# Optimization experiments

Measured on AMD Instinct MI355X. Metric: run time of the kernel, lower is better.

Reference implementation:

```python
import jax, jax.numpy as jnp
import numpy as np

B, T, D, H, L = 2, 1000, 768, 12, 2
DK = D // H
MLP_HID = D * 1  # mlp_ratio = 1
WIDTHS = [7, 15, 31, 63, 127, 255, 7, 15, 31, 63, 127, 255]


def _band_mask():
    # diagonal_mask(seq_len, mask_width): True = blocked (outside the diagonal band)
    i = np.arange(T)[:, None]
    j = np.arange(T)[None, :]
    m = np.stack([np.abs(i - j) > (w // 2) for w in WIDTHS], 0)  # (H, T, T)
    return jnp.asarray(m)


def _rel_pos_emb():
    # espnet-style RelPositionalEncoding: rel positions T-1 .. -(T-1), shape (2T-1, D)
    pos = jnp.arange(T - 1, -T, -1, dtype=jnp.float32)
    div = jnp.exp(jnp.arange(0, D, 2, dtype=jnp.float32) * (-np.log(10000.0) / D))
    ang = pos[:, None] * div[None, :]
    return jnp.stack([jnp.sin(ang), jnp.cos(ang)], -1).reshape(2 * T - 1, D)


def setup_inputs() -> dict:
    key = jax.random.key(0)
    ks = iter(jax.random.split(key, 32))
    rn = lambda sh, s=0.02: jax.random.normal(next(ks), sh, jnp.float32) * s
    return {
        "x": jax.random.normal(next(ks), (B, T, D), jnp.float32),
        "mask": _band_mask(),
        "ln1_g": jnp.ones((L, D)), "ln1_b": jnp.zeros((L, D)),
        "wq": rn((L, D, D)), "bq": jnp.zeros((L, D)),
        "wk": rn((L, D, D)), "bk": jnp.zeros((L, D)),
        "wv": rn((L, D, D)), "bv": jnp.zeros((L, D)),
        "wo": rn((L, D, D)), "bo": jnp.zeros((L, D)),
        "wpos": rn((L, D, D)),
        "pbu": rn((L, H, DK)), "pbv": rn((L, H, DK)),
        "ln2_g": jnp.ones((L, D)), "ln2_b": jnp.zeros((L, D)),
        "w1": rn((L, D, MLP_HID)), "b1": jnp.zeros((L, MLP_HID)),
        "w2": rn((L, MLP_HID, D)), "b2": jnp.zeros((L, D)),
    }


def _ln(x, g, b):
    m = jnp.mean(x, -1, keepdims=True)
    v = jnp.var(x, -1, keepdims=True)
    return (x - m) * jax.lax.rsqrt(v + 1e-5) * g + b


def _rel_shift(x):
    # x: (b, h, t, 2t-1) -> shifted so column s corresponds to rel pos (t-1 - s + row offset)
    b, h, t, n = x.shape
    x = jnp.pad(x, ((0, 0), (0, 0), (0, 0), (1, 0)))        # (b,h,t,2t)
    x = x.reshape(b, h, n + 1, t)[:, :, 1:, :].reshape(b, h, t, n)
    return x[..., :t]


def _forward(x, mask, p):
    (ln1_g, ln1_b, wq, bq, wk, bk, wv, bv, wo, bo,
     wpos, pbu, pbv, ln2_g, ln2_b, w1, b1, w2, b2) = p
    pe = _rel_pos_emb()                                      # (2T-1, D)
    x = x * jnp.asarray(np.sqrt(D), x.dtype)                 # xscale in RelPositionalEncoding
    neg = jnp.asarray(-1e30, x.dtype)
    inv_sqrt_dk = 1.0 / np.sqrt(DK)
    for l in range(L):
        h = _ln(x, ln1_g[l], ln1_b[l])
        q = (h @ wq[l] + bq[l]).reshape(B, T, H, DK)
        k = (h @ wk[l] + bk[l]).reshape(B, T, H, DK)
        v = (h @ wv[l] + bv[l]).reshape(B, T, H, DK)
        pp = (pe @ wpos[l]).reshape(2 * T - 1, H, DK)        # pos projection (no bias)
        ac = jnp.einsum('bthd,bshd->bhts', q + pbu[l], k)    # content term
        bd = _rel_shift(jnp.einsum('bthd,nhd->bhtn', q + pbv[l], pp))  # position term
        s = (ac + bd) * inv_sqrt_dk
        s = jnp.where(mask[None], neg, s)                    # per-head diagonal band mask
        a = jax.nn.softmax(s, axis=-1)
        o = jnp.einsum('bhts,bshd->bthd', a, v).reshape(B, T, D) @ wo[l] + bo[l]
        x = x + o
        h2 = _ln(x, ln2_g[l], ln2_b[l])
        x = x + (jax.nn.gelu(h2 @ w1[l] + b1[l], approximate=False) @ w2[l] + b2[l])
    return x


def reference(x, mask, ln1_g, ln1_b, wq, bq, wk, bk, wv, bv, wo, bo, wpos, pbu, pbv, ln2_g, ln2_b, w1, b1, w2, b2):
    return _forward(x, mask, (ln1_g, ln1_b, wq, bq, wk, bk, wv, bv, wo, bo,
                              wpos, pbu, pbv, ln2_g, ln2_b, w1, b1, w2, b2))
```

## Files before the change

kernel.cpp:

```cpp
#include <hip/hip_runtime.h>

#define TT 1000
#define BB 2
#define DD 768
#define HH 12
#define DK 64
#define LL 2
#define WELEM 589824
#define PEROWS 255
#define VTP 1312
#define PPL 195840

typedef __bf16 bf16x8 __attribute__((ext_vector_type(8)));
typedef float floatx4 __attribute__((ext_vector_type(4)));

__device__ __constant__ int HALFW[12] = {3,7,15,31,63,127,3,7,15,31,63,127};
__device__ __constant__ int HORD[12]  = {5,11,4,10,3,9,2,8,1,7,0,6};


__device__ __forceinline__ float b2f(unsigned short u){
    union { unsigned int i; float f; } x; x.i = ((unsigned int)u) << 16; return x.f;
}
__device__ __forceinline__ unsigned short f2b(float f){
    union { float f; unsigned int i; } x; x.f = f;
    unsigned int i = x.i;
    i += 0x7fffu + ((i >> 16) & 1u);
    return (unsigned short)(i >> 16);
}
__device__ __forceinline__ void gload16(const void* g, void* l){
    __builtin_amdgcn_global_load_lds(
        (const __attribute__((address_space(1))) void*)g,
        (__attribute__((address_space(3))) void*)l, 16, 0, 0);
}

__global__ __launch_bounds__(256)
void prep_kernel(const float* s0, const float* s1, const float* s2, const float* s3,
                 const float* s4, const float* s5, const float* s6,
                 unsigned short* __restrict__ dst,
                 const float* __restrict__ x, float* __restrict__ xc,
                 unsigned short* __restrict__ pe,
                 const float* __restrict__ lg0, const float* __restrict__ lb0,
                 unsigned short* __restrict__ ln0out){
    int z = blockIdx.z;
    int tid = threadIdx.x;
    if (z < 14){
        const float* srcs[7] = {s0,s1,s2,s3,s4,s5,s6};
        const float* src = srcs[z % 7] + (size_t)(z / 7)*WELEM;
        unsigned short* d = dst + (size_t)z*WELEM;
        int k0 = blockIdx.x*64, n0 = blockIdx.y*64;
        __shared__ __align__(16) unsigned short tile[64][72];
        int r = tid >> 2, c = tid & 3;
        const float4* sp = (const float4*)(src + (size_t)(k0+r)*DD + n0 + c*16);
        float4 f0 = sp[0], f1 = sp[1], f2 = sp[2], f3 = sp[3];
        unsigned short u[16];
        u[0]=f2b(f0.x); u[1]=f2b(f0.y); u[2]=f2b(f0.z); u[3]=f2b(f0.w);
        u[4]=f2b(f1.x); u[5]=f2b(f1.y); u[6]=f2b(f1.z); u[7]=f2b(f1.w);
        u[8]=f2b(f2.x); u[9]=f2b(f2.y); u[10]=f2b(f2.z); u[11]=f2b(f2.w);
        u[12]=f2b(f3.x); u[13]=f2b(f3.y); u[14]=f2b(f3.z); u[15]=f2b(f3.w);
        *(int4*)&tile[r][c*16]   = *(int4*)&u[0];
        *(int4*)&tile[r][c*16+8] = *(int4*)&u[8];
        __syncthreads();
        unsigned short tmp[16];
        #pragma unroll
        for (int i=0;i<16;++i) tmp[i] = tile[c*16+i][r];
        int4* dp = (int4*)(d + (size_t)(n0+r)*DD + k0 + c*16);
        dp[0] = *(int4*)&tmp[0];
        dp[1] = *(int4*)&tmp[8];
    } else if (z == 14){
        int bid = blockIdx.y*12 + blockIdx.x;
        int wv = tid>>6, lane = tid&63;
        const float SCL = 27.712812921102035f;
        #pragma unroll
        for (int it = 0; it < 4; ++it){
            int rr = it*4 + wv;
            if (rr < 14){
                int row = bid*14 + rr;
                if (row < 2000){
                    const float4* xr = (const float4*)x + (size_t)row*192;
                    float4* xcr = (float4*)xc + (size_t)row*192;
                    float4 vv[3];
                    float s = 0.f, ss = 0.f;
                    #pragma unroll
                    for (int j=0;j<3;++j){
                        float4 vq = xr[lane + 64*j];
                        vq.x *= SCL; vq.y *= SCL; vq.z *= SCL; vq.w *= SCL;
                        vv[j] = vq;
                        s  += vq.x+vq.y+vq.z+vq.w;
                        ss += vq.x*vq.x+vq.y*vq.y+vq.z*vq.z+vq.w*vq.w;
                        xcr[lane + 64*j] = vq;
                    }
                    #pragma unroll
                    for (int o=1;o<64;o<<=1){ s += __shfl_xor(s,o); ss += __shfl_xor(ss,o); }
                    float mean = s*(1.0f/768.0f);
                    float var  = ss*(1.0f/768.0f) - mean*mean;
                    float inv  = 1.0f/sqrtf(var + 1e-5f);
                    unsigned short* orow = ln0out + (size_t)row*768;
                    #pragma unroll
                    for (int j=0;j<3;++j){
                        int i0 = (lane + 64*j)*4;
                        unsigned short o4[4];
                        o4[0] = f2b((vv[j].x-mean)*inv*lg0[i0]   + lb0[i0]);
                        o4[1] = f2b((vv[j].y-mean)*inv*lg0[i0+1] + lb0[i0+1]);
                        o4[2] = f2b((vv[j].z-mean)*inv*lg0[i0+2] + lb0[i0+2]);
                        o4[3] = f2b((vv[j].w-mean)*inv*lg0[i0+3] + lb0[i0+3]);
                        *(unsigned long long*)&orow[i0] = *(unsigned long long*)o4;
                    }
                }
            }
        }
    } else {
        int bid = blockIdx.y*12 + blockIdx.x;
        #pragma unroll
        for (int rr = 0; rr < 2; ++rr){
            int row = bid*2 + rr;
            if (row < PEROWS){
                float pos = (float)(127 - row);
                int i = tid;
                float dv = expf((float)(2*i) * (-9.210340371976184f / 768.0f));
                float ang = pos * dv;
                pe[(size_t)row*DD + 2*i]   = f2b(sinf(ang));
                pe[(size_t)row*DD + 2*i+1] = f2b(cosf(ang));
                if (tid < 128){
                    int j = 256 + tid;
                    float dv2 = expf((float)(2*j) * (-9.210340371976184f / 768.0f));
                    float an2 = pos * dv2;
                    pe[(size_t)row*DD + 2*j]   = f2b(sinf(an2));
                    pe[(size_t)row*DD + 2*j+1] = f2b(cosf(an2));
                }
            }
        }
    }
}

__global__ __launch_bounds__(256)
void ln_kernel(const float* __restrict__ x, const float* __restrict__ g,
               const float* __restrict__ bb, unsigned short* __restrict__ out){
    int row = blockIdx.x;
    const float* xr = x + (size_t)row*DD;
    int tid = threadIdx.x;
    float v0 = xr[tid], v1 = xr[tid+256], v2 = xr[tid+512];
    float s = v0+v1+v2, ss = v0*v0+v1*v1+v2*v2;
    #pragma unroll
    for (int o=1;o<64;o<<=1){ s += __shfl_xor(s,o); ss += __shfl_xor(ss,o); }
    __shared__ float rs[4], rss[4];
    int wv = tid>>6, lane = tid&63;
    if (lane==0){ rs[wv]=s; rss[wv]=ss; }
    __syncthreads();
    s  = rs[0]+rs[1]+rs[2]+rs[3];
    ss = rss[0]+rss[1]+rss[2]+rss[3];
    float mean = s * (1.0f/768.0f);
    float var  = ss * (1.0f/768.0f) - mean*mean;
    float inv  = 1.0f / sqrtf(var + 1e-5f);
    unsigned short* orow = out + (size_t)row*DD;
    #pragma unroll
    for (int kk=0;kk<3;++kk){
        int i = tid + 256*kk;
        float v = (kk==0?v0:(kk==1?v1:v2));
        orow[i] = f2b((v - mean)*inv*g[i] + bb[i]);
    }
}

#define GEMM_GL64(A_, Bt_, M0_, n0_, M_)                                        \
    int tid = threadIdx.x;                                                      \
    int m0 = (M0_);                                                             \
    int wv = tid>>6, lane = tid&63;                                             \
    int quad = lane>>4, l16 = lane&15;                                          \
    floatx4 acc[4];                                                             \
    _Pragma("unroll")                                                           \
    for (int ni=0;ni<4;++ni) acc[ni] = (floatx4){0.f,0.f,0.f,0.f};              \
    {                                                                           \
      int rl0 = wv*16 + (lane>>3);                                              \
      int rl1 = rl0 + 8;                                                        \
      int gc  = (lane&7) ^ (lane>>3);                                           \
      int ra0 = m0 + rl0; if (ra0 > (M_)-1) ra0 = (M_)-1;                       \
      int ra1 = m0 + rl1; if (ra1 > (M_)-1) ra1 = (M_)-1;                       \
      const char* gA0 = (const char*)(A_)  + (size_t)ra0*1536 + gc*16;          \
      const char* gA1 = (const char*)(A_)  + (size_t)ra1*1536 + gc*16;          \
      const char* gB0 = (const char*)(Bt_) + (size_t)((n0_)+rl0)*1536 + gc*16;  \
      const char* gB1 = (const char*)(Bt_) + (size_t)((n0_)+rl1)*1536 + gc*16;  \
      char* shB = (char*)sh;                                                    \
      int ld0 = (2*wv)*1024, ld1 = (2*wv+1)*1024;                               \
      int arow = (16*wv + l16)*64;                                              \
      int sw8  = l16 & 7;                                                       \
      int cq0 = (quad ^ sw8)*8;                                                 \
      int cq1 = ((4|quad) ^ sw8)*8;                                             \
      gload16(gA0, shB + ld0);                                                  \
      gload16(gA1, shB + ld1);                                                  \
      gload16(gB0, shB + 8192 + ld0);                                           \
      gload16(gB1, shB + 8192 + ld1);                                           \
      for (int s=0; s<12; ++s){                                                 \
        if (s < 11){                                                            \
          char* nb = shB + ((s+1)&1)*16384;                                     \
          int off = (s+1)*128;                                                  \
          gload16(gA0 + off, nb + ld0);                                         \
          gload16(gA1 + off, nb + ld1);                                         \
          gload16(gB0 + off, nb + 8192 + ld0);                                  \
          gload16(gB1 + off, nb + 8192 + ld1);                                  \
          asm volatile("s_waitcnt vmcnt(4)" ::: "memory");                      \
        } else {                                                                \
          asm volatile("s_waitcnt vmcnt(0)" ::: "memory");                      \
        }                                                                       \
        __builtin_amdgcn_s_barrier();                                           \
        __builtin_amdgcn_sched_barrier(0);                                      \
        const unsigned short* cA = sh + (s&1)*8192;                             \
        const unsigned short* cB = cA + 4096;                                   \
        _Pragma("unroll")                                                       \
        for (int kh=0; kh<2; ++kh){                                             \
          int cq = kh ? cq1 : cq0;                                              \
          bf16x8 af = *(const bf16x8*)&cA[arow + cq];                           \
          _Pragma("unroll")                                                     \
          for (int ni=0; ni<4; ++ni){                                           \
            bf16x8 bfv = *(const bf16x8*)&cB[ni*1024 + l16*64 + cq];            \
            acc[ni] = __builtin_amdgcn_mfma_f32_16x16x32_bf16(af, bfv, acc[ni], 0,0,0); \
          }                                                                     \
        }                                                                       \
        __builtin_amdgcn_sched_barrier(0);                                      \
        __builtin_amdgcn_s_barrier();                                           \
      }                                                                         \
    }

#define GEMM_GL64_3B(A_, Bt_, M0_, n0_, M_)                                     \
    int tid = threadIdx.x;                                                      \
    int m0 = (M0_);                                                             \
    int wv = tid>>6, lane = tid&63;                                             \
    int quad = lane>>4, l16 = lane&15;                                          \
    floatx4 acc[4];                                                             \
    _Pragma("unroll")                                                           \
    for (int ni=0;ni<4;++ni) acc[ni] = (floatx4){0.f,0.f,0.f,0.f};              \
    {                                                                           \
      int rl0 = wv*16 + (lane>>3);                                              \
      int rl1 = rl0 + 8;                                                        \
      int gc  = (lane&7) ^ (lane>>3);                                           \
      int ra0 = m0 + rl0; if (ra0 > (M_)-1) ra0 = (M_)-1;                       \
      int ra1 = m0 + rl1; if (ra1 > (M_)-1) ra1 = (M_)-1;                       \
      const char* gA0 = (const char*)(A_)  + (size_t)ra0*1536 + gc*16;          \
      const char* gA1 = (const char*)(A_)  + (size_t)ra1*1536 + gc*16;          \
      const char* gB0 = (const char*)(Bt_) + (size_t)((n0_)+rl0)*1536 + gc*16;  \
      const char* gB1 = (const char*)(Bt_) + (size_t)((n0_)+rl1)*1536 + gc*16;  \
      char* shB = (char*)sh;                                                    \
      int ld0 = (2*wv)*1024, ld1 = (2*wv+1)*1024;                               \
      int arow = (16*wv + l16)*64;                                              \
      int sw8  = l16 & 7;                                                       \
      int cq0 = (quad ^ sw8)*8;                                                 \
      int cq1 = ((4|quad) ^ sw8)*8;                                             \
      gload16(gA0, shB + ld0);                                                  \
      gload16(gA1, shB + ld1);                                                  \
      gload16(gB0, shB + 8192 + ld0);                                           \
      gload16(gB1, shB + 8192 + ld1);                                           \
      gload16(gA0 + 128, shB + 16384 + ld0);                                    \
      gload16(gA1 + 128, shB + 16384 + ld1);                                    \
      gload16(gB0 + 128, shB + 16384 + 8192 + ld0);                             \
      gload16(gB1 + 128, shB + 16384 + 8192 + ld1);                             \
      for (int s=0; s<12; ++s){                                                 \
        if (s < 11) asm volatile("s_waitcnt vmcnt(4)" ::: "memory");            \
        else        asm volatile("s_waitcnt vmcnt(0)" ::: "memory");            \
        __builtin_amdgcn_s_barrier();                                           \
        __builtin_amdgcn_sched_barrier(0);                                      \
        if (s < 10){                                                            \
          char* nb = shB + ((s+2)%3)*16384;                                     \
          int off = (s+2)*128;                                                  \
          gload16(gA0 + off, nb + ld0);                                         \
          gload16(gA1 + off, nb + ld1);                                         \
          gload16(gB0 + off, nb + 8192 + ld0);                                  \
          gload16(gB1 + off, nb + 8192 + ld1);                                  \
        }                                                                       \
        __builtin_amdgcn_sched_barrier(0);                                      \
        const unsigned short* cA = sh + (s%3)*8192;                             \
        const unsigned short* cB = cA + 4096;                                   \
        _Pragma("unroll")                                                       \
        for (int kh=0; kh<2; ++kh){                                             \
          int cq = kh ? cq1 : cq0;                                              \
          bf16x8 af = *(const bf16x8*)&cA[arow + cq];                           \
          _Pragma("unroll")                                                     \
          for (int ni=0; ni<4; ++ni){                                           \
            bf16x8 bfv = *(const bf16x8*)&cB[ni*1024 + l16*64 + cq];            \
            acc[ni] = __builtin_amdgcn_mfma_f32_16x16x32_bf16(af, bfv, acc[ni], 0,0,0); \
          }                                                                     \
        }                                                                       \
        __builtin_amdgcn_sched_barrier(0);                                      \
      }                                                                         \
    }

template<int MODE>
__global__ __launch_bounds__(256)
void gemm_kernel(const unsigned short* __restrict__ A, const unsigned short* __restrict__ Bt,
                 const float* __restrict__ bias, unsigned short* __restrict__ outb,
                 float* __restrict__ resid, int M){
    __shared__ __align__(16) unsigned short sh[24576];
    int n0 = blockIdx.y*64;
    GEMM_GL64_3B(A, Bt, blockIdx.x*64, n0, M)
    float bfv_[4];
    #pragma unroll
    for (int ni=0;ni<4;++ni) bfv_[ni] = bias ? bias[n0 + 16*ni + l16] : 0.0f;
    #pragma unroll
    for (int rr=0;rr<4;++rr){
        int row = m0 + 16*wv + 4*quad + rr;
        if (row >= M) continue;
        #pragma unroll
        for (int ni=0;ni<4;++ni){
            int col = n0 + 16*ni + l16;
            float v = acc[ni][rr] + bfv_[ni];
            if (MODE == 1)      outb[(size_t)row*768 + col] = f2b(0.5f*v*(1.0f + erff(v*0.70710678118654752f)));
            else                resid[(size_t)row*768 + col] += v;
        }
    }
}

__global__ __launch_bounds__(256)
void gemm_qkv_kernel(const unsigned short* __restrict__ A, const unsigned short* __restrict__ Bt,
                     const float* __restrict__ bq, const float* __restrict__ bk, const float* __restrict__ bv,
                     unsigned short* __restrict__ qout, unsigned short* __restrict__ kout,
                     unsigned short* __restrict__ vout,
                     const unsigned short* __restrict__ peA, const unsigned short* __restrict__ posBt,
                     unsigned short* __restrict__ ppout){
    __shared__ __align__(16) unsigned short sh[16384];
    int bid = blockIdx.x;
    if (bid < 1152){
        int ny = bid >> 5;
        int n0 = ny * 64;
        GEMM_GL64(A, Bt, (bid & 31)*64, n0, 2000)
        int sec = ny / 12;
        int col0 = n0 - sec*768;
        int h = col0 >> 6;
        const float* bias = (sec==0) ? bq : (sec==1) ? bk : bv;
        float bfv_[4];
        #pragma unroll
        for (int ni=0;ni<4;++ni) bfv_[ni] = bias[col0 + 16*ni + l16];
        if (sec != 2){
            unsigned short* outp = (sec==0) ? qout : kout;
            #pragma unroll
            for (int rr=0;rr<4;++rr){
                int row = m0 + 16*wv + 4*quad + rr;
                if (row >= 2000) continue;
                int b = row / TT, tl = row - b*TT;
                #pragma unroll
                for (int ni=0;ni<4;++ni){
                    int d = 16*ni + l16;
                    outp[(((size_t)(b*HH + h))*TT + tl)*DK + d] = f2b(acc[ni][rr] + bfv_[ni]);
                }
            }
        } else {
            #pragma unroll
            for (int rr=0;rr<4;++rr){
                int rt = 16*wv + 4*quad + rr;
                #pragma unroll
                for (int ni=0;ni<4;++ni)
                    sh[rt*66 + 16*ni + l16] = f2b(acc[ni][rr] + bfv_[ni]);
            }
            __syncthreads();
            #pragma unroll
            for (int it=0; it<16; ++it){
                int idx = it*256 + tid;
                int d = idx >> 6, rt = idx & 63;
                int row = m0 + rt;
                if (row < 2000){
                    int b = row / TT, tl = row - b*TT;
                    vout[(((size_t)(b*HH + h))*DK + d)*VTP + tl + 128] = sh[rt*66 + d];
                }
            }
        }
    } else {
        int pid = bid - 1152;
        int pz = pid / 48, rem = pid % 48;
        int pn0 = (rem >> 2) * 64;
        const unsigned short* Bt_ = posBt + (size_t)pz*7*WELEM;
        unsigned short* outb_ = ppout + (size_t)pz*PPL;
        GEMM_GL64(peA, Bt_, (rem & 3)*64, pn0, PEROWS)
        #pragma unroll
        for (int rr=0;rr<4;++rr){
            int row = m0 + 16*wv + 4*quad + rr;
            if (row >= PEROWS) continue;
            #pragma unroll
            for (int ni=0;ni<4;++ni){
                int col = pn0 + 16*ni + l16;
                int h = col >> 6, d = col & 63;
                outb_[((size_t)h*PEROWS + row)*DK + d] = f2b(acc[ni][rr]);
            }
        }
    }
}

__global__ __launch_bounds__(256)
void attn_kernel(const unsigned short* __restrict__ q, const unsigned short* __restrict__ k,
                 const unsigned short* __restrict__ vT, const unsigned short* __restrict__ pp,
                 const float* __restrict__ pbu, const float* __restrict__ pbv,
                 unsigned short* __restrict__ out){
    int b = blockIdx.y, h = HORD[blockIdx.z];
    int t0 = blockIdx.x * 16;
    int w2 = HALFW[h];
    int tid = threadIdx.x;
    int wv = tid >> 6, lane = tid & 63;
    int l16 = lane & 15, quad = lane >> 4;

    const unsigned short* qB = q  + ((size_t)(b*HH + h))*TT*DK;
    const unsigned short* kB = k  + ((size_t)(b*HH + h))*TT*DK;
    const unsigned short* vB = vT + ((size_t)(b*HH + h))*DK*VTP;
    const unsigned short* pB = pp + (size_t)h*PEROWS*DK;

    __shared__ __align__(16) float bd[16*260];
    __shared__ __align__(16) unsigned short pl[16*328];
    __shared__ float sms[4][16];

    int tq = t0 + l16; if (tq > TT-1) tq = TT-1;
    union { int4 i; unsigned short u[8]; } r0, r1;
    r0.i = *(const int4*)(qB + (size_t)tq*DK + quad*8);
    r1.i = *(const int4*)(qB + (size_t)tq*DK + 32 + quad*8);
    const float* pu = pbu + h*DK + quad*8;
    const float* pv = pbv + h*DK + quad*8;
    union { unsigned short u[8]; bf16x8 v; } qu0, qu1, qv0, qv1;
    #pragma unroll
    for (int i=0;i<8;++i){
        float a0 = b2f(r0.u[i]), a1 = b2f(r1.u[i]);
        qu0.u[i] = f2b(a0 + pu[i]);
        qu1.u[i] = f2b(a1 + pu[32+i]);
        qv0.u[i] = f2b(a0 + pv[i]);
        qv1.u[i] = f2b(a1 + pv[32+i]);
    }

    int Nn = 2*w2 + 1;
    int ntiles = (Nn + 15) >> 4;
    for (int ti = wv; ti < ntiles; ti += 4){
        int n = 127 - w2 + ti*16 + l16; if (n > PEROWS-1) n = PEROWS-1;
        const unsigned short* pr = pB + (size_t)n*DK + quad*8;
        bf16x8 pb0 = *(const bf16x8*)pr;
        bf16x8 pb1 = *(const bf16x8*)(pr + 32);
        floatx4 a = {0.f,0.f,0.f,0.f};
        a = __builtin_amdgcn_mfma_f32_16x16x32_bf16(qv0.v, pb0, a, 0,0,0);
        a = __builtin_amdgcn_mfma_f32_16x16x32_bf16(qv1.v, pb1, a, 0,0,0);
        #pragma unroll
        for (int r=0;r<4;++r) bd[(quad*4+r)*260 + ti*16 + l16] = a[r];
    }
    for (int i = tid; i < 16*328/4; i += 256)
        ((unsigned long long*)pl)[i] = 0ULL;
    __syncthreads();

    int Ns = 2*w2 + 16;
    int stiles = (Ns + 15) >> 4;
    int s_lo = t0 - w2;
    float scv[5][4];
    #pragma unroll
    for (int ii = 0; ii < 5; ++ii){
        int ti = wv + ii*4;
        if (ti < stiles){
            int s = s_lo + ti*16 + l16;
            int sc = s < 0 ? 0 : (s > TT-1 ? TT-1 : s);
            const unsigned short* kr = kB + (size_t)sc*DK + quad*8;
            bf16x8 kb0 = *(const bf16x8*)kr;
            bf16x8 kb1 = *(const bf16x8*)(kr + 32);
            floatx4 a = {0.f,0.f,0.f,0.f};
            a = __builtin_amdgcn_mfma_f32_16x16x32_bf16(qu0.v, kb0, a, 0,0,0);
            a = __builtin_amdgcn_mfma_f32_16x16x32_bf16(qu1.v, kb1, a, 0,0,0);
            #pragma unroll
            for (int r=0;r<4;++r){
                int row = quad*4 + r;
                int nrel = ti*16 + l16 - row;
                bool ok = (nrel >= 0) && (nrel <= 2*w2) && (s >= 0) && (s <= TT-1);
                int idx = row*260 + nrel;
                idx = idx < 0 ? 0 : (idx > 16*260-1 ? 16*260-1 : idx);
                float bdv = bd[idx];
                scv[ii][r] = ok ? (a[r] + bdv) * 0.125f : -1e30f;
            }
        } else {
            #pragma unroll
            for (int r=0;r<4;++r) scv[ii][r] = -1e30f;
        }
    }

    float sm[4] = {0.f,0.f,0.f,0.f};
    #pragma unroll
    for (int ii = 0; ii < 5; ++ii){
        int ti = wv + ii*4;
        if (ti < stiles){
            int pad_base = (t0 - w2) - ((t0 - w2) & ~31);
            #pragma unroll
            for (int r=0;r<4;++r){
                float e = __expf(scv[ii][r]);
                sm[r] += e;
                pl[(quad*4+r)*328 + pad_base + ti*16 + l16] = f2b(e);
            }
        }
    }
    #pragma unroll
    for (int off=1; off<16; off<<=1){
        #pragma unroll
        for (int r=0;r<4;++r) sm[r] += __shfl_xor(sm[r], off);
    }
    if (l16 == 0){
        #pragma unroll
        for (int r=0;r<4;++r) sms[wv][quad*4+r] = sm[r];
    }
    __syncthreads();

    int s_lo2 = t0 - w2;
    int s0a = s_lo2 & ~31;
    int pad_lo = s_lo2 - s0a;
    int ktiles = (pad_lo + Ns + 31) >> 5;

    floatx4 oacc = {0.f,0.f,0.f,0.f};
    for (int kt = 0; kt < ktiles; ++kt){
        bf16x8 pa = *(const bf16x8*)&pl[l16*328 + kt*32 + quad*8];
        int sidx = s0a + kt*32 + quad*8 + 128;
        bf16x8 vb = *(const bf16x8*)(vB + (size_t)(wv*16 + l16)*VTP + sidx);
        oacc = __builtin_amdgcn_mfma_f32_16x16x32_bf16(pa, vb, oacc, 0,0,0);
    }
    #pragma unroll
    for (int r=0;r<4;++r){
        int row = quad*4 + r;
        float sum = sms[0][row] + sms[1][row] + sms[2][row] + sms[3][row];
        float rinv = sum > 0.f ? 1.0f/sum : 0.0f;
        int t = t0 + row;
        if (t <= TT-1)
            out[(((size_t)(b*TT + t))*HH + h)*DK + wv*16 + l16] = f2b(oacc[r] * rinv);
    }
}

extern "C" void kernel_launch(void* const* d_in, const int* in_sizes, int n_in,
                              void* d_out, int out_size, void* d_ws, size_t ws_size,
                              hipStream_t stream){
    const float* x    = (const float*)d_in[0];
    const float* ln1g = (const float*)d_in[2];
    const float* ln1b = (const float*)d_in[3];
    const float* wq   = (const float*)d_in[4];
    const float* bq   = (const float*)d_in[5];
    const float* wk   = (const float*)d_in[6];
    const float* bk   = (const float*)d_in[7];
    const float* wvv  = (const float*)d_in[8];
    const float* bv   = (const float*)d_in[9];
    const float* wo   = (const float*)d_in[10];
    const float* bo   = (const float*)d_in[11];
    const float* wpos = (const float*)d_in[12];
    const float* pbu  = (const float*)d_in[13];
    const float* pbv  = (const float*)d_in[14];
    const float* ln2g = (const float*)d_in[15];
    const float* ln2b = (const float*)d_in[16];
    const float* w1   = (const float*)d_in[17];
    const float* b1   = (const float*)d_in[18];
    const float* w2   = (const float*)d_in[19];
    const float* b2   = (const float*)d_in[20];

    const int NTOK = BB*TT;

    float* x_cur = (float*)d_out;

    char* ws = (char*)d_ws;
    unsigned short* qbuf  = (unsigned short*)(ws);
    unsigned short* kbuf  = (unsigned short*)(ws + 3072000);
    unsigned short* vTbuf = (unsigned short*)(ws + 6144000);
    unsigned short* hbuf  = (unsigned short*)(ws + 10174464);
    unsigned short* ppbuf = (unsigned short*)(ws + 13246464);
    unsigned short* pebuf = (unsigned short*)(ws + 14029824);
    unsigned short* wtbuf = (unsigned short*)(ws + 14421504);
    #define WT(t_,l_) (wtbuf + (size_t)((l_)*7 + (t_))*WELEM)

    dim3 blk(256);
    prep_kernel<<<dim3(12,12,16), blk, 0, stream>>>(wq, wk, wvv, wo, wpos, w1, w2,
                                                    wtbuf, x, x_cur, pebuf,
                                                    ln1g, ln1b, hbuf);

    dim3 gBig(32, 12);
    dim3 gAttn(63, BB, HH);

    for (int l = 0; l < LL; ++l){
        long dl = (long)l*DD;
        long pl_ = (long)l*HH*DK;

        if (l == 1)
            ln_kernel<<<NTOK, blk, 0, stream>>>(x_cur, ln1g + dl, ln1b + dl, hbuf);

        int nqkv = (l == 0) ? 1248 : 1152;
        gemm_qkv_kernel<<<dim3(nqkv), blk, 0, stream>>>(hbuf, WT(0,l), bq + dl, bk + dl, bv + dl,
                                                        qbuf, kbuf, vTbuf,
                                                        pebuf, WT(4,0), ppbuf);

        attn_kernel<<<gAttn, blk, 0, stream>>>(qbuf, kbuf, vTbuf, ppbuf + (size_t)l*PPL,
                                               pbu + pl_, pbv + pl_, hbuf);

        gemm_kernel<2><<<gBig, blk, 0, stream>>>(hbuf, WT(3,l), bo + dl, nullptr, x_cur, NTOK);

        ln_kernel<<<NTOK, blk, 0, stream>>>(x_cur, ln2g + dl, ln2b + dl, hbuf);
        gemm_kernel<1><<<gBig, blk, 0, stream>>>(hbuf, WT(5,l), b1 + dl, qbuf, nullptr, NTOK);
        gemm_kernel<2><<<gBig, blk, 0, stream>>>(qbuf, WT(6,l), b2 + dl, nullptr, x_cur, NTOK);
    }
}
```

Before: 276.7 us.

## Fold LayerNorm2 into residual GEMM epilogue and FC1 weights via row stats

```diff
diff --git a/kernel.cpp b/kernel.cpp
--- a/kernel.cpp
+++ b/kernel.cpp
@@ -40,7 +40,8 @@
                  const float* __restrict__ x, float* __restrict__ xc,
                  unsigned short* __restrict__ pe,
                  const float* __restrict__ lg0, const float* __restrict__ lb0,
-                 unsigned short* __restrict__ ln0out){
+                 unsigned short* __restrict__ ln0out,
+                 const float* __restrict__ g2){
     int z = blockIdx.z;
     int tid = threadIdx.x;
     if (z < 14){
@@ -52,6 +53,13 @@
         int r = tid >> 2, c = tid & 3;
         const float4* sp = (const float4*)(src + (size_t)(k0+r)*DD + n0 + c*16);
         float4 f0 = sp[0], f1 = sp[1], f2 = sp[2], f3 = sp[3];
+        if (z % 7 == 5){
+            float g = g2[(size_t)(z/7)*DD + k0 + r];
+            f0.x*=g; f0.y*=g; f0.z*=g; f0.w*=g;
+            f1.x*=g; f1.y*=g; f1.z*=g; f1.w*=g;
+            f2.x*=g; f2.y*=g; f2.z*=g; f2.w*=g;
+            f3.x*=g; f3.y*=g; f3.z*=g; f3.w*=g;
+        }
         unsigned short u[16];
         u[0]=f2b(f0.x); u[1]=f2b(f0.y); u[2]=f2b(f0.z); u[3]=f2b(f0.w);
         u[4]=f2b(f1.x); u[5]=f2b(f1.y); u[6]=f2b(f1.z); u[7]=f2b(f1.w);
@@ -285,23 +293,57 @@
 __global__ __launch_bounds__(256)
 void gemm_kernel(const unsigned short* __restrict__ A, const unsigned short* __restrict__ Bt,
                  const float* __restrict__ bias, unsigned short* __restrict__ outb,
-                 float* __restrict__ resid, int M){
+                 float* __restrict__ resid, int M,
+                 float* __restrict__ stats, unsigned short* __restrict__ xbf,
+                 const float* __restrict__ uv, const float* __restrict__ cv){
     __shared__ __align__(16) unsigned short sh[24576];
     int n0 = blockIdx.y*64;
     GEMM_GL64_3B(A, Bt, blockIdx.x*64, n0, M)
     float bfv_[4];
     #pragma unroll
     for (int ni=0;ni<4;++ni) bfv_[ni] = bias ? bias[n0 + 16*ni + l16] : 0.0f;
-    #pragma unroll
-    for (int rr=0;rr<4;++rr){
-        int row = m0 + 16*wv + 4*quad + rr;
-        if (row >= M) continue;
-        #pragma unroll
-        for (int ni=0;ni<4;++ni){
-            int col = n0 + 16*ni + l16;
-            float v = acc[ni][rr] + bfv_[ni];
-            if (MODE == 1)      outb[(size_t)row*768 + col] = f2b(0.5f*v*(1.0f + erff(v*0.70710678118654752f)));
-            else                resid[(size_t)row*768 + col] += v;
+    if (MODE == 1){
+        float un[4], cn[4];
+        #pragma unroll
+        for (int ni=0;ni<4;++ni){ int col = n0 + 16*ni + l16; un[ni] = uv[col]; cn[ni] = cv[col]; }
+        #pragma unroll
+        for (int rr=0;rr<4;++rr){
+            int row = m0 + 16*wv + 4*quad + rr;
+            if (row >= M) continue;
+            float sum = stats[row*2], ssq = stats[row*2+1];
+            float mean = sum*(1.0f/768.0f);
+            float var  = ssq*(1.0f/768.0f) - mean*mean;
+            float inv  = 1.0f/sqrtf(var + 1e-5f);
+            float im   = -inv*mean;
+            #pragma unroll
+            for (int ni=0;ni<4;++ni){
+                int col = n0 + 16*ni + l16;
+                float v = inv*acc[ni][rr] + im*un[ni] + cn[ni] + bfv_[ni];
+                outb[(size_t)row*768 + col] = f2b(0.5f*v*(1.0f + erff(v*0.70710678118654752f)));
+            }
+        }
+    } else {
+        #pragma unroll
+        for (int rr=0;rr<4;++rr){
+            int row = m0 + 16*wv + 4*quad + rr;
+            if (row >= M) continue;
+            float sp = 0.f, ssp = 0.f;
+            #pragma unroll
+            for (int ni=0;ni<4;++ni){
+                int col = n0 + 16*ni + l16;
+                size_t idx = (size_t)row*768 + col;
+                float rn = resid[idx] + acc[ni][rr] + bfv_[ni];
+                resid[idx] = rn;
+                if (stats){ xbf[idx] = f2b(rn); sp += rn; ssp += rn*rn; }
+            }
+            if (stats){
+                #pragma unroll
+                for (int off=1; off<16; off<<=1){ sp += __shfl_xor(sp,off); ssp += __shfl_xor(ssp,off); }
+                if (l16 == 0){
+                    atomicAdd(stats + row*2,     sp);
+                    atomicAdd(stats + row*2 + 1, ssp);
+                }
+            }
         }
     }
 }
@@ -384,13 +426,37 @@
 void attn_kernel(const unsigned short* __restrict__ q, const unsigned short* __restrict__ k,
                  const unsigned short* __restrict__ vT, const unsigned short* __restrict__ pp,
                  const float* __restrict__ pbu, const float* __restrict__ pbv,
-                 unsigned short* __restrict__ out){
+                 unsigned short* __restrict__ out,
+                 const float* __restrict__ w1f, const float* __restrict__ g2,
+                 const float* __restrict__ b2l, float* __restrict__ statz,
+                 float* __restrict__ uc){
     int b = blockIdx.y, h = HORD[blockIdx.z];
     int t0 = blockIdx.x * 16;
     int w2 = HALFW[h];
     int tid = threadIdx.x;
     int wv = tid >> 6, lane = tid & 63;
     int l16 = lane & 15, quad = lane >> 4;
+
+    if (statz && blockIdx.x == 0){
+        int aux = blockIdx.y*12 + blockIdx.z;
+        for (int i = aux*256 + tid; i < 8000; i += 6144) statz[i] = 0.f;
+        if (tid < 64){
+            int t = aux*64 + tid;
+            int mat = (t >= 768) ? 1 : 0;
+            int n = t - mat*768;
+            const float* wp = w1f + (size_t)mat*WELEM + n;
+            const float* gp = g2  + (size_t)mat*DD;
+            const float* bp = b2l + (size_t)mat*DD;
+            float ua = 0.f, ca = 0.f;
+            #pragma unroll 4
+            for (int kk = 0; kk < 768; ++kk){
+                float w = wp[(size_t)kk*768];
+                ua += gp[kk]*w;
+                ca += bp[kk]*w;
+            }
+            uc[t] = ua; uc[1536 + t] = ca;
+        }
+    }
 
     const unsigned short* qB = q  + ((size_t)(b*HH + h))*TT*DK;
     const unsigned short* kB = k  + ((size_t)(b*HH + h))*TT*DK;
@@ -550,12 +616,15 @@
     unsigned short* ppbuf = (unsigned short*)(ws + 13246464);
     unsigned short* pebuf = (unsigned short*)(ws + 14029824);
     unsigned short* wtbuf = (unsigned short*)(ws + 14421504);
+    float* statsb = (float*)pebuf;
+    float* ucb    = (float*)pebuf + 8000;
+    unsigned short* xbf = vTbuf;
     #define WT(t_,l_) (wtbuf + (size_t)((l_)*7 + (t_))*WELEM)
 
     dim3 blk(256);
     prep_kernel<<<dim3(12,12,16), blk, 0, stream>>>(wq, wk, wvv, wo, wpos, w1, w2,
                                                     wtbuf, x, x_cur, pebuf,
-                                                    ln1g, ln1b, hbuf);
+                                                    ln1g, ln1b, hbuf, ln2g);
 
     dim3 gBig(32, 12);
     dim3 gAttn(63, BB, HH);
@@ -573,12 +642,18 @@
                                                         pebuf, WT(4,0), ppbuf);
 
         attn_kernel<<<gAttn, blk, 0, stream>>>(qbuf, kbuf, vTbuf, ppbuf + (size_t)l*PPL,
-                                               pbu + pl_, pbv + pl_, hbuf);
-
-        gemm_kernel<2><<<gBig, blk, 0, stream>>>(hbuf, WT(3,l), bo + dl, nullptr, x_cur, NTOK);
-
-        ln_kernel<<<NTOK, blk, 0, stream>>>(x_cur, ln2g + dl, ln2b + dl, hbuf);
-        gemm_kernel<1><<<gBig, blk, 0, stream>>>(hbuf, WT(5,l), b1 + dl, qbuf, nullptr, NTOK);
-        gemm_kernel<2><<<gBig, blk, 0, stream>>>(qbuf, WT(6,l), b2 + dl, nullptr, x_cur, NTOK);
-    }
-}
+                                               pbu + pl_, pbv + pl_, hbuf,
+                                               w1, ln2g, ln2b,
+                                               (l == 0) ? statsb : nullptr, ucb);
+
+        gemm_kernel<2><<<gBig, blk, 0, stream>>>(hbuf, WT(3,l), bo + dl, nullptr, x_cur, NTOK,
+                                                 statsb + l*4000, xbf, nullptr, nullptr);
+
+        gemm_kernel<1><<<gBig, blk, 0, stream>>>(xbf, WT(5,l), b1 + dl, qbuf, nullptr, NTOK,
+                                                 statsb + l*4000, nullptr,
+                                                 ucb + l*768, ucb + 1536 + l*768);
+
+        gemm_kernel<2><<<gBig, blk, 0, stream>>>(qbuf, WT(6,l), b2 + dl, nullptr, x_cur, NTOK,
+                                                 nullptr, nullptr, nullptr, nullptr);
+    }
+}
```

Result: slower. 340.9 us (+23.2%).
